# Kernel optimization log

Hardware: AMD Instinct MI355X
Metric: run time of the kernel (lower is better)

Reference implementation:

```python
import jax, jax.numpy as jnp
import numpy as np

EPS = 1e-5

def _layer_norm(x, gamma, beta):
    # LayerNorm over the last two dims [C, 128], matching nn.LayerNorm([C, 128])
    mean = jnp.mean(x, axis=(-2, -1), keepdims=True)
    var = jnp.var(x, axis=(-2, -1), keepdims=True)
    return (x - mean) * jax.lax.rsqrt(var + EPS) * gamma + beta


def setup_inputs() -> dict:
    key = jax.random.key(0)
    ks = jax.random.split(key, 7)
    B, C, N, L = 64, 1024, 128, 512
    W_SCALE = 0.02  # keep pre-softmax logits / activations in a sane range
    return {
        "X_in": jax.random.normal(ks[0], (B, C, N), jnp.float32),
        "T": jax.random.normal(ks[1], (B, C, L), jnp.float32),
        "Wq": jax.random.normal(ks[2], (C, C), jnp.float32) * W_SCALE,
        "Wk": jax.random.normal(ks[3], (C, C), jnp.float32) * W_SCALE,
        "Wv": jax.random.normal(ks[4], (C, C), jnp.float32) * W_SCALE,
        "Wf1": jax.random.normal(ks[5], (C, C), jnp.float32) * W_SCALE,
        "Wf2": jax.random.normal(ks[6], (C, C), jnp.float32) * W_SCALE,
        "gamma": jnp.ones((C, N), jnp.float32),
        "beta": jnp.zeros((C, N), jnp.float32),
    }


def reference(X_in, T, Wq, Wk, Wv, Wf1, Wf2, gamma, beta):
    C = Wq.shape[1]  # feature_map_cs (intended value of the buggy X_in.weight.shape[1])
    # 1x1 Conv1d == per-position channel matmul: weight [out, in]
    q = jnp.einsum('oc,bcn->bon', Wq, X_in)      # [B, C, N]
    k = jnp.einsum('oc,bcl->bol', Wk, T)         # [B, C, L]
    sim = jnp.einsum('bcn,bcl->bnl', q, k) / jnp.sqrt(jnp.float32(C))  # [B, N, L]
    attn = jax.nn.softmax(sim, axis=2)           # softmax over tokens L
    v = jnp.einsum('oc,bcl->bol', Wv, T)         # [B, C, L]
    ctx = jnp.einsum('bcl,bnl->bcn', v, attn)    # [B, C, N] == bmm(values, attn^T)
    X_out = _layer_norm(X_in + ctx, gamma, beta)
    h = jax.nn.relu(jnp.einsum('oc,bcn->bon', Wf1, X_out))
    ffn = jnp.einsum('oc,bcn->bon', Wf2, h)
    return _layer_norm(X_out + ffn, gamma, beta)
```

## Files before the change

### kernel.cpp

```cpp
#include <hip/hip_runtime.h>


using bf16   = __bf16;
using bf16x2 = __attribute__((ext_vector_type(2))) __bf16;
using bf16x4 = __attribute__((ext_vector_type(4))) __bf16;
using bf16x8 = __attribute__((ext_vector_type(8))) __bf16;
using f32x4  = __attribute__((ext_vector_type(4))) float;

static constexpr int  Bb = 64;
static constexpr int  Cc = 1024;
static constexpr int  Nn = 128;
static constexpr int  Ll = 512;
static constexpr long long PLANE = (long long)Cc * Nn;
static constexpr float INV_PLANE = 1.0f / 131072.0f;

__device__ __forceinline__ void gload_lds16(const void* g, void* l) {
    __builtin_amdgcn_global_load_lds(
        (__attribute__((address_space(1))) void*)g,
        (__attribute__((address_space(3))) void*)l,
        16, 0, 0);
}

__global__ void cast_w3(const float* __restrict__ a, const float* __restrict__ b,
                        const float* __restrict__ c,
                        bf16* __restrict__ oa, bf16* __restrict__ ob, bf16* __restrict__ oc) {
    const float* in; bf16* out;
    switch (blockIdx.y) {
        case 0: in = a; out = oa; break;
        case 1: in = b; out = ob; break;
        default: in = c; out = oc; break;
    }
    int i = blockIdx.x * 256 + threadIdx.x;
    float4 v = reinterpret_cast<const float4*>(in)[i];
    bf16x4 o = { (bf16)v.x, (bf16)v.y, (bf16)v.z, (bf16)v.w };
    reinterpret_cast<bf16x4*>(out)[i] = o;
}

template <bool DUAL>
__global__ void transpose_cast_f(const float* __restrict__ in, bf16* __restrict__ outT,
                                 bf16* __restrict__ outS, int R, int S) {
    __shared__ float tile[64][65];
    long long plane = (long long)R * S;
    in   += (long long)blockIdx.z * plane;
    outT += (long long)blockIdx.z * plane;
    if (DUAL) outS += (long long)blockIdx.z * plane;
    int s0 = blockIdx.x * 64, r0 = blockIdx.y * 64;
    int t = threadIdx.x;
    int rl = t >> 4;
    int sc = (t & 15) * 4;
    #pragma unroll
    for (int p = 0; p < 4; ++p) {
        int r = p * 16 + rl;
        float4 v = *(const float4*)(in + (long long)(r0 + r) * S + s0 + sc);
        *(float4*)&tile[r][sc] = v;
        if (DUAL) {
            bf16x4 o = { (bf16)v.x, (bf16)v.y, (bf16)v.z, (bf16)v.w };
            *(bf16x4*)(outS + (long long)(r0 + r) * S + s0 + sc) = o;
        }
    }
    __syncthreads();
    int sb = t >> 3;
    int rg = (t & 7) * 8;
    #pragma unroll
    for (int p = 0; p < 2; ++p) {
        int s = sb + p * 32;
        bf16x8 o;
        #pragma unroll
        for (int j = 0; j < 8; ++j) o[j] = (bf16)tile[rg + j][s];
        *(bf16x8*)(outT + (long long)(s0 + s) * R + r0 + rg) = o;
    }
}

#define GEMM_PROLOGUE_AND_LOOP(A_, Bt_, K_)                                        \
    __shared__ bf16 As[128 * 64];                                                  \
    __shared__ bf16 Bs[128 * 64];                                                  \
    const int n0   = blockIdx.x * 128;                                             \
    const int m0   = blockIdx.y * 128;                                             \
    const int t    = threadIdx.x;                                                  \
    const int lane = t & 63;                                                       \
    const int w    = t >> 6;                                                       \
    const int wr   = (w >> 1) * 64;                                                \
    const int wc   = (w & 1) * 64;                                                 \
    const int lr   = lane & 15;                                                    \
    const int hi4  = (lane >> 4) * 16;                                             \
    const int sw   = (lr & 7) << 4;                                                \
    const bf16* gA[4]; const bf16* gB[4]; int lo[4];                               \
    _Pragma("unroll")                                                              \
    for (int p = 0; p < 4; ++p) {                                                  \
        int o = w * 1024 + lane * 16 + p * 4096;                                   \
        int row = o >> 7;                                                          \
        int scol = ((o & 127) ^ ((row & 7) << 4)) >> 1;                            \
        lo[p] = o;                                                                 \
        gA[p] = A_  + (long long)(m0 + row) * K_ + scol;                           \
        gB[p] = Bt_ + (long long)(n0 + row) * K_ + scol;                           \
    }                                                                              \
    f32x4 acc[4][4] = {};                                                          \
    for (int k0 = 0; k0 < K_; k0 += 64) {                                          \
        _Pragma("unroll")                                                          \
        for (int p = 0; p < 4; ++p) gload_lds16(gA[p] + k0, (char*)As + lo[p]);    \
        _Pragma("unroll")                                                          \
        for (int p = 0; p < 4; ++p) gload_lds16(gB[p] + k0, (char*)Bs + lo[p]);    \
        __syncthreads();                                                           \
        _Pragma("unroll")                                                          \
        for (int kk = 0; kk < 2; ++kk) {                                           \
            bf16x8 af[4], bfr[4];                                                  \
            _Pragma("unroll")                                                      \
            for (int i = 0; i < 4; ++i) {                                          \
                int ra = wr + i * 16 + lr;                                         \
                int rb = wc + i * 16 + lr;                                         \
                af[i]  = *(const bf16x8*)((const char*)As +                        \
                          ((((ra << 7) + (kk << 6) + hi4)) ^ sw));                 \
                bfr[i] = *(const bf16x8*)((const char*)Bs +                        \
                          ((((rb << 7) + (kk << 6) + hi4)) ^ sw));                 \
            }                                                                      \
            _Pragma("unroll")                                                      \
            for (int mi = 0; mi < 4; ++mi)                                         \
                _Pragma("unroll")                                                  \
                for (int ni = 0; ni < 4; ++ni)                                     \
                    acc[mi][ni] = __builtin_amdgcn_mfma_f32_16x16x32_bf16(         \
                        af[mi], bfr[ni], acc[mi][ni], 0, 0, 0);                    \
        }                                                                          \
        __syncthreads();                                                           \
    }

template <typename OutT, bool RELU>
__global__ void __launch_bounds__(256, 2)
gemm_tn(const bf16* __restrict__ A, const bf16* __restrict__ Bt, OutT* __restrict__ C,
        int M, int N, int K, long long sA, long long sBt, long long sC, float scale) {
    A  += (long long)blockIdx.z * sA;
    Bt += (long long)blockIdx.z * sBt;
    C  += (long long)blockIdx.z * sC;
    GEMM_PROLOGUE_AND_LOOP(A, Bt, K)
    const int rbase = m0 + wr + (lane >> 4) * 4;
    const int cbase = n0 + wc + lr;
    #pragma unroll
    for (int mi = 0; mi < 4; ++mi)
        #pragma unroll
        for (int ni = 0; ni < 4; ++ni)
            #pragma unroll
            for (int r = 0; r < 4; ++r) {
                float v = acc[mi][ni][r] * scale;
                if (RELU) v = fmaxf(v, 0.0f);
                C[(long long)(rbase + mi * 16 + r) * N + (cbase + ni * 16)] = (OutT)v;
            }
}

__global__ void __launch_bounds__(256, 2)
gemm_ctx_ln1(const bf16* __restrict__ A , const bf16* __restrict__ Bt ,
             const float* __restrict__ X, float* __restrict__ Z1, float* __restrict__ partials,
             int K, long long sBt) {
    const int N = Nn;
    Bt += (long long)blockIdx.z * sBt;
    X  += (long long)blockIdx.z * PLANE;
    Z1 += (long long)blockIdx.z * PLANE;
    GEMM_PROLOGUE_AND_LOOP(A, Bt, K)
    const int rbase = m0 + wr + (lane >> 4) * 4;
    const int cbase = n0 + wc + lr;
    float s = 0.f, ss = 0.f;
    #pragma unroll
    for (int mi = 0; mi < 4; ++mi)
        #pragma unroll
        for (int ni = 0; ni < 4; ++ni)
            #pragma unroll
            for (int r = 0; r < 4; ++r) {
                long long idx = (long long)(rbase + mi * 16 + r) * N + (cbase + ni * 16);
                float zv = acc[mi][ni][r] + X[idx];
                Z1[idx] = zv;
                s += zv; ss += zv * zv;
            }
    #pragma unroll
    for (int off = 32; off; off >>= 1) { s += __shfl_xor(s, off); ss += __shfl_xor(ss, off); }
    __shared__ float red[8];
    if (lane == 0) { red[w] = s; red[4 + w] = ss; }
    __syncthreads();
    if (t == 0) {
        float S = red[0] + red[1] + red[2] + red[3];
        float SS = red[4] + red[5] + red[6] + red[7];
        float* p = partials + ((long long)blockIdx.z * 8 + blockIdx.y) * 2;
        p[0] = S; p[1] = SS;
    }
}

__global__ void __launch_bounds__(256, 2)
gemm_ffn_ln2(const bf16* __restrict__ A , const bf16* __restrict__ Bt ,
             const float* __restrict__ Xout, float* __restrict__ Z2, float* __restrict__ partials,
             int K, long long sA) {
    A    += (long long)blockIdx.z * sA;
    Xout += (long long)blockIdx.z * PLANE;
    Z2   += (long long)blockIdx.z * PLANE;
    GEMM_PROLOGUE_AND_LOOP(A, Bt, K)
    const int rbase = m0 + wr + (lane >> 4) * 4;
    const int cbase = n0 + wc + lr;
    float s = 0.f, ss = 0.f;
    #pragma unroll
    for (int mi = 0; mi < 4; ++mi)
        #pragma unroll
        for (int ni = 0; ni < 4; ++ni) {
            long long a = (long long)(cbase + ni * 16) * Nn + rbase + mi * 16;
            float4 xo = *(const float4*)(Xout + a);
            float4 zv = { acc[mi][ni][0] + xo.x, acc[mi][ni][1] + xo.y,
                          acc[mi][ni][2] + xo.z, acc[mi][ni][3] + xo.w };
            *(float4*)(Z2 + a) = zv;
            s  += zv.x + zv.y + zv.z + zv.w;
            ss += zv.x * zv.x + zv.y * zv.y + zv.z * zv.z + zv.w * zv.w;
        }
    #pragma unroll
    for (int off = 32; off; off >>= 1) { s += __shfl_xor(s, off); ss += __shfl_xor(ss, off); }
    __shared__ float red[8];
    if (lane == 0) { red[w] = s; red[4 + w] = ss; }
    __syncthreads();
    if (t == 0) {
        float S = red[0] + red[1] + red[2] + red[3];
        float SS = red[4] + red[5] + red[6] + red[7];
        float* p = partials + ((long long)blockIdx.z * 8 + blockIdx.x) * 2;
        p[0] = S; p[1] = SS;
    }
}

__global__ void softmax_rows_512(const float* __restrict__ sim, bf16* __restrict__ attn) {
    int row  = blockIdx.x * 4 + (threadIdx.x >> 6);
    int lane = threadIdx.x & 63;
    const float* p = sim + (long long)row * Ll + lane * 8;
    float4 a = *(const float4*)p;
    float4 b = *(const float4*)(p + 4);
    float v[8] = {a.x, a.y, a.z, a.w, b.x, b.y, b.z, b.w};
    float mx = v[0];
    #pragma unroll
    for (int j = 1; j < 8; ++j) mx = fmaxf(mx, v[j]);
    #pragma unroll
    for (int off = 32; off; off >>= 1) mx = fmaxf(mx, __shfl_xor(mx, off));
    float s = 0.f;
    #pragma unroll
    for (int j = 0; j < 8; ++j) { v[j] = __expf(v[j] - mx); s += v[j]; }
    #pragma unroll
    for (int off = 32; off; off >>= 1) s += __shfl_xor(s, off);
    float inv = 1.f / s;
    bf16x8 o;
    #pragma unroll
    for (int j = 0; j < 8; ++j) o[j] = (bf16)(v[j] * inv);
    *(bf16x8*)(attn + (long long)row * Ll + lane * 8) = o;
}

__global__ void ln1_norm_transpose(const float* __restrict__ Z1, const float* __restrict__ partials,
                                   const float* __restrict__ gamma, const float* __restrict__ beta,
                                   float* __restrict__ Xout, bf16* __restrict__ XoutT) {
    int b = blockIdx.z;
    float S = 0.f, SS = 0.f;
    #pragma unroll
    for (int j = 0; j < 8; ++j) {
        S  += partials[((long long)b * 8 + j) * 2];
        SS += partials[((long long)b * 8 + j) * 2 + 1];
    }
    float mean = S * INV_PLANE;
    float var  = SS * INV_PLANE - mean * mean;
    float rstd = rsqrtf(var + 1e-5f);
    __shared__ float tile[64][65];
    long long base = (long long)b * PLANE;
    int n0 = blockIdx.x * 64, c0 = blockIdx.y * 64;
    int t = threadIdx.x;
    int rl = t >> 4;
    int sc = (t & 15) * 4;
    #pragma unroll
    for (int p = 0; p < 4; ++p) {
        int r = p * 16 + rl;
        long long idx = (long long)(c0 + r) * Nn + n0 + sc;
        float4 z  = *(const float4*)(Z1 + base + idx);
        float4 g  = *(const float4*)(gamma + idx);
        float4 be = *(const float4*)(beta + idx);
        float4 o = {(z.x - mean) * rstd * g.x + be.x, (z.y - mean) * rstd * g.y + be.y,
                    (z.z - mean) * rstd * g.z + be.z, (z.w - mean) * rstd * g.w + be.w};
        *(float4*)(Xout + base + idx) = o;
        *(float4*)&tile[r][sc] = o;
    }
    __syncthreads();
    int sb = t >> 3;
    int rg = (t & 7) * 8;
    #pragma unroll
    for (int p = 0; p < 2; ++p) {
        int n = sb + p * 32;
        bf16x8 o;
        #pragma unroll
        for (int j = 0; j < 8; ++j) o[j] = (bf16)tile[rg + j][n];
        *(bf16x8*)(XoutT + base + (long long)(n0 + n) * Cc + c0 + rg) = o;
    }
}

__global__ void ln2_final(const float* __restrict__ Z2, const float* __restrict__ partials,
                          const float* __restrict__ gamma, const float* __restrict__ beta,
                          float* __restrict__ out) {
    int b = blockIdx.y;
    float S = 0.f, SS = 0.f;
    #pragma unroll
    for (int j = 0; j < 8; ++j) {
        S  += partials[((long long)b * 8 + j) * 2];
        SS += partials[((long long)b * 8 + j) * 2 + 1];
    }
    float mean = S * INV_PLANE;
    float var  = SS * INV_PLANE - mean * mean;
    float rstd = rsqrtf(var + 1e-5f);
    long long base = (long long)b * PLANE;
    int i = (blockIdx.x * 256 + threadIdx.x) * 4;
    float4 z  = *(const float4*)(Z2 + base + i);
    float4 g  = *(const float4*)(gamma + i);
    float4 be = *(const float4*)(beta + i);
    float4 o = {(z.x - mean) * rstd * g.x + be.x, (z.y - mean) * rstd * g.y + be.y,
                (z.z - mean) * rstd * g.z + be.z, (z.w - mean) * rstd * g.w + be.w};
    *(float4*)(out + base + i) = o;
}

extern "C" void kernel_launch(void* const* d_in, const int* in_sizes, int n_in,
                              void* d_out, int out_size, void* d_ws, size_t ws_size,
                              hipStream_t stream) {
    const float* X   = (const float*)d_in[0];
    const float* T   = (const float*)d_in[1];
    const float* Wq  = (const float*)d_in[2];
    const float* Wk  = (const float*)d_in[3];
    const float* Wv  = (const float*)d_in[4];
    const float* Wf1 = (const float*)d_in[5];
    const float* Wf2 = (const float*)d_in[6];
    const float* gamma = (const float*)d_in[7];
    const float* beta  = (const float*)d_in[8];
    float* out = (float*)d_out;
    char* ws = (char*)d_ws;
    const size_t MB = 1ull << 20;

    bf16* WvB  = (bf16*)(ws + 0 * MB);
    bf16* Wf1B = (bf16*)(ws + 2 * MB);
    bf16* Wf2B = (bf16*)(ws + 4 * MB);
    bf16* WqT  = (bf16*)(ws + 6 * MB);
    bf16* WkT  = (bf16*)(ws + 8 * MB);
    bf16* G2   = (bf16*)(ws + 10 * MB);
    bf16* Xt   = (bf16*)(ws + 12 * MB);
    bf16* Tt   = (bf16*)(ws + 28 * MB);
    float* Z1  = (float*)(ws + 28 * MB);
    float* Xout= (float*)(ws + 60 * MB);
    bf16* Tb   = (bf16*)(ws + 92 * MB);
    bf16* XoutT= (bf16*)(ws + 92 * MB);
    bf16* hT   = (bf16*)(ws + 108 * MB);
    bf16* e    = (bf16*)(ws + 156 * MB);
    float* Z2  = (float*)(ws + 156 * MB);
    float* sim = (float*)(ws + 172 * MB);
    bf16* attn = (bf16*)(ws + 188 * MB);
    bf16* u    = (bf16*)(ws + 196 * MB);
    float* pp1 = (float*)(ws + 212 * MB);
    float* pp2 = (float*)(ws + 212 * MB + 65536);

    dim3 blk256(256);

    cast_w3<<<dim3(Cc * Cc / 4 / 256, 3), blk256, 0, stream>>>(
        Wv, Wf1, Wf2, WvB, Wf1B, Wf2B);
    transpose_cast_f<false><<<dim3(16, 16, 1), blk256, 0, stream>>>(Wq, WqT, nullptr, Cc, Cc);
    transpose_cast_f<false><<<dim3(16, 16, 1), blk256, 0, stream>>>(Wk, WkT, nullptr, Cc, Cc);
    transpose_cast_f<false><<<dim3(Nn / 64, Cc / 64, Bb), blk256, 0, stream>>>(X, Xt, nullptr, Cc, Nn);
    transpose_cast_f<true><<<dim3(Ll / 64, Cc / 64, Bb), blk256, 0, stream>>>(T, Tt, Tb, Cc, Ll);

    gemm_tn<bf16, false><<<dim3(8, 8, 1), blk256, 0, stream>>>(
        WkT, WqT, G2, Cc, Cc, Cc, 0, 0, 0, 1.f);
    gemm_tn<bf16, false><<<dim3(8, 1, Bb), blk256, 0, stream>>>(
        Xt, G2, e, Nn, Cc, Cc, (long long)Nn * Cc, 0, (long long)Nn * Cc, 1.f);
    gemm_tn<float, false><<<dim3(4, 1, Bb), blk256, 0, stream>>>(
        e, Tt, sim, Nn, Ll, Cc, (long long)Nn * Cc, (long long)Ll * Cc,
        (long long)Nn * Ll, 0.03125f);
    softmax_rows_512<<<dim3(Bb * Nn / 4), blk256, 0, stream>>>(sim, attn);
    gemm_tn<bf16, false><<<dim3(8, 1, Bb), blk256, 0, stream>>>(
        attn, Tb, u, Nn, Cc, Ll, (long long)Nn * Ll, (long long)Cc * Ll,
        (long long)Nn * Cc, 1.f);
    gemm_ctx_ln1<<<dim3(1, 8, Bb), blk256, 0, stream>>>(
        WvB, u, X, Z1, pp1, Cc, (long long)Nn * Cc);
    ln1_norm_transpose<<<dim3(Nn / 64, Cc / 64, Bb), blk256, 0, stream>>>(
        Z1, pp1, gamma, beta, Xout, XoutT);
    gemm_tn<bf16, true><<<dim3(8, 1, Bb), blk256, 0, stream>>>(
        XoutT, Wf1B, hT, Nn, Cc, Cc, (long long)Nn * Cc, 0, (long long)Nn * Cc, 1.f);
    gemm_ffn_ln2<<<dim3(8, 1, Bb), blk256, 0, stream>>>(
        hT, Wf2B, Xout, Z2, pp2, Cc, (long long)Nn * Cc);
    ln2_final<<<dim3(128, Bb), blk256, 0, stream>>>(Z2, pp2, gamma, beta, out);
}
```

Baseline: 303.8 us.

## Fuse softmax into sim GEMM epilogue and recompute LN1 inside FFN2

The sim GEMM now writes exp(logits) as bf16 plus per-block row-sum partials, and the attention-value GEMM applies the reciprocal row sum in its epilogue. This removes the fp32 sim buffer and the separate softmax kernel. The fp32 Xout buffer is no longer written; the FFN2 epilogue recomputes LayerNorm-1 from Z1 and the stats. The Wq/Wk transposes are merged into one launch. Dropping max subtraction risks exp overflow for large logits.

```diff
diff --git a/kernel.cpp b/kernel.cpp
--- a/kernel.cpp
+++ b/kernel.cpp
@@ -68,6 +68,32 @@
         #pragma unroll
         for (int j = 0; j < 8; ++j) o[j] = (bf16)tile[rg + j][s];
         *(bf16x8*)(outT + (long long)(s0 + s) * R + r0 + rg) = o;
+    }
+}
+
+__global__ void transpose_cast_w2(const float* __restrict__ a, bf16* __restrict__ oa,
+                                  const float* __restrict__ b, bf16* __restrict__ ob) {
+    __shared__ float tile[64][65];
+    const float* in = blockIdx.z ? b : a;
+    bf16* out       = blockIdx.z ? ob : oa;
+    int s0 = blockIdx.x * 64, r0 = blockIdx.y * 64;
+    int t = threadIdx.x;
+    int rl = t >> 4, sc = (t & 15) * 4;
+    #pragma unroll
+    for (int p = 0; p < 4; ++p) {
+        int r = p * 16 + rl;
+        float4 v = *(const float4*)(in + (long long)(r0 + r) * Cc + s0 + sc);
+        *(float4*)&tile[r][sc] = v;
+    }
+    __syncthreads();
+    int sb = t >> 3, rg = (t & 7) * 8;
+    #pragma unroll
+    for (int p = 0; p < 2; ++p) {
+        int s = sb + p * 32;
+        bf16x8 o;
+        #pragma unroll
+        for (int j = 0; j < 8; ++j) o[j] = (bf16)tile[rg + j][s];
+        *(bf16x8*)(out + (long long)(s0 + s) * Cc + r0 + rg) = o;
     }
 }
 
@@ -146,6 +172,76 @@
 }
 
 __global__ void __launch_bounds__(256, 2)
+gemm_sim_exp(const bf16* __restrict__ A , const bf16* __restrict__ Bt ,
+             bf16* __restrict__ E, float* __restrict__ rspart, int K,
+             long long sA, long long sBt) {
+    A  += (long long)blockIdx.z * sA;
+    Bt += (long long)blockIdx.z * sBt;
+    E  += (long long)blockIdx.z * ((long long)Nn * Ll);
+    GEMM_PROLOGUE_AND_LOOP(A, Bt, K)
+    const int rbase = m0 + wr + (lane >> 4) * 4;
+    const int cbase = n0 + wc + lr;
+    __shared__ float rs[2][128];
+    float psum[4][4];
+    #pragma unroll
+    for (int mi = 0; mi < 4; ++mi)
+        #pragma unroll
+        for (int r = 0; r < 4; ++r) psum[mi][r] = 0.f;
+    #pragma unroll
+    for (int mi = 0; mi < 4; ++mi)
+        #pragma unroll
+        for (int ni = 0; ni < 4; ++ni)
+            #pragma unroll
+            for (int r = 0; r < 4; ++r) {
+                float ev = __expf(acc[mi][ni][r] * 0.03125f);
+                E[(long long)(rbase + mi * 16 + r) * Ll + (cbase + ni * 16)] = (bf16)ev;
+                psum[mi][r] += ev;
+            }
+    #pragma unroll
+    for (int mi = 0; mi < 4; ++mi)
+        #pragma unroll
+        for (int r = 0; r < 4; ++r) {
+            float v = psum[mi][r];
+            v += __shfl_xor(v, 1); v += __shfl_xor(v, 2);
+            v += __shfl_xor(v, 4); v += __shfl_xor(v, 8);
+            psum[mi][r] = v;
+        }
+    if (lr == 0) {
+        #pragma unroll
+        for (int mi = 0; mi < 4; ++mi)
+            #pragma unroll
+            for (int r = 0; r < 4; ++r)
+                rs[wc ? 1 : 0][wr + (lane >> 4) * 4 + mi * 16 + r] = psum[mi][r];
+    }
+    __syncthreads();
+    if (t < 128)
+        rspart[((long long)blockIdx.z * 4 + blockIdx.x) * 128 + t] = rs[0][t] + rs[1][t];
+}
+
+__global__ void __launch_bounds__(256, 2)
+gemm_u_scaled(const bf16* __restrict__ A , const bf16* __restrict__ Bt ,
+              bf16* __restrict__ C, const float* __restrict__ rspart, int K,
+              long long sA, long long sBt, long long sC) {
+    A  += (long long)blockIdx.z * sA;
+    Bt += (long long)blockIdx.z * sBt;
+    C  += (long long)blockIdx.z * sC;
+    const float* rp = rspart + (long long)blockIdx.z * 512;
+    GEMM_PROLOGUE_AND_LOOP(A, Bt, K)
+    const int rbase = m0 + wr + (lane >> 4) * 4;
+    const int cbase = n0 + wc + lr;
+    #pragma unroll
+    for (int mi = 0; mi < 4; ++mi)
+        #pragma unroll
+        for (int r = 0; r < 4; ++r) {
+            int row = rbase + mi * 16 + r;
+            float inv = 1.f / (rp[row] + rp[128 + row] + rp[256 + row] + rp[384 + row]);
+            #pragma unroll
+            for (int ni = 0; ni < 4; ++ni)
+                C[(long long)row * Cc + (cbase + ni * 16)] = (bf16)(acc[mi][ni][r] * inv);
+        }
+}
+
+__global__ void __launch_bounds__(256, 2)
 gemm_ctx_ln1(const bf16* __restrict__ A , const bf16* __restrict__ Bt ,
              const float* __restrict__ X, float* __restrict__ Z1, float* __restrict__ partials,
              int K, long long sBt) {
@@ -183,11 +279,21 @@
 
 __global__ void __launch_bounds__(256, 2)
 gemm_ffn_ln2(const bf16* __restrict__ A , const bf16* __restrict__ Bt ,
-             const float* __restrict__ Xout, float* __restrict__ Z2, float* __restrict__ partials,
+             const float* __restrict__ Z1, const float* __restrict__ pp1,
+             const float* __restrict__ gamma, const float* __restrict__ beta,
+             float* __restrict__ Z2, float* __restrict__ partials,
              int K, long long sA) {
-    A    += (long long)blockIdx.z * sA;
-    Xout += (long long)blockIdx.z * PLANE;
-    Z2   += (long long)blockIdx.z * PLANE;
+    A  += (long long)blockIdx.z * sA;
+    Z1 += (long long)blockIdx.z * PLANE;
+    Z2 += (long long)blockIdx.z * PLANE;
+    float S1 = 0.f, SS1 = 0.f;
+    #pragma unroll
+    for (int j = 0; j < 8; ++j) {
+        S1  += pp1[((long long)blockIdx.z * 8 + j) * 2];
+        SS1 += pp1[((long long)blockIdx.z * 8 + j) * 2 + 1];
+    }
+    const float mean1 = S1 * INV_PLANE;
+    const float rstd1 = rsqrtf(SS1 * INV_PLANE - mean1 * mean1 + 1e-5f);
     GEMM_PROLOGUE_AND_LOOP(A, Bt, K)
     const int rbase = m0 + wr + (lane >> 4) * 4;
     const int cbase = n0 + wc + lr;
@@ -197,7 +303,13 @@
         #pragma unroll
         for (int ni = 0; ni < 4; ++ni) {
             long long a = (long long)(cbase + ni * 16) * Nn + rbase + mi * 16;
-            float4 xo = *(const float4*)(Xout + a);
+            float4 z1v = *(const float4*)(Z1 + a);
+            float4 g  = *(const float4*)(gamma + a);
+            float4 be = *(const float4*)(beta + a);
+            float4 xo = {(z1v.x - mean1) * rstd1 * g.x + be.x,
+                         (z1v.y - mean1) * rstd1 * g.y + be.y,
+                         (z1v.z - mean1) * rstd1 * g.z + be.z,
+                         (z1v.w - mean1) * rstd1 * g.w + be.w};
             float4 zv = { acc[mi][ni][0] + xo.x, acc[mi][ni][1] + xo.y,
                           acc[mi][ni][2] + xo.z, acc[mi][ni][3] + xo.w };
             *(float4*)(Z2 + a) = zv;
@@ -217,33 +329,9 @@
     }
 }
 
-__global__ void softmax_rows_512(const float* __restrict__ sim, bf16* __restrict__ attn) {
-    int row  = blockIdx.x * 4 + (threadIdx.x >> 6);
-    int lane = threadIdx.x & 63;
-    const float* p = sim + (long long)row * Ll + lane * 8;
-    float4 a = *(const float4*)p;
-    float4 b = *(const float4*)(p + 4);
-    float v[8] = {a.x, a.y, a.z, a.w, b.x, b.y, b.z, b.w};
-    float mx = v[0];
-    #pragma unroll
-    for (int j = 1; j < 8; ++j) mx = fmaxf(mx, v[j]);
-    #pragma unroll
-    for (int off = 32; off; off >>= 1) mx = fmaxf(mx, __shfl_xor(mx, off));
-    float s = 0.f;
-    #pragma unroll
-    for (int j = 0; j < 8; ++j) { v[j] = __expf(v[j] - mx); s += v[j]; }
-    #pragma unroll
-    for (int off = 32; off; off >>= 1) s += __shfl_xor(s, off);
-    float inv = 1.f / s;
-    bf16x8 o;
-    #pragma unroll
-    for (int j = 0; j < 8; ++j) o[j] = (bf16)(v[j] * inv);
-    *(bf16x8*)(attn + (long long)row * Ll + lane * 8) = o;
-}
-
 __global__ void ln1_norm_transpose(const float* __restrict__ Z1, const float* __restrict__ partials,
                                    const float* __restrict__ gamma, const float* __restrict__ beta,
-                                   float* __restrict__ Xout, bf16* __restrict__ XoutT) {
+                                   bf16* __restrict__ XoutT) {
     int b = blockIdx.z;
     float S = 0.f, SS = 0.f;
     #pragma unroll
@@ -269,7 +357,6 @@
         float4 be = *(const float4*)(beta + idx);
         float4 o = {(z.x - mean) * rstd * g.x + be.x, (z.y - mean) * rstd * g.y + be.y,
                     (z.z - mean) * rstd * g.z + be.z, (z.w - mean) * rstd * g.w + be.w};
-        *(float4*)(Xout + base + idx) = o;
         *(float4*)&tile[r][sc] = o;
     }
     __syncthreads();
@@ -333,24 +420,22 @@
     bf16* Xt   = (bf16*)(ws + 12 * MB);
     bf16* Tt   = (bf16*)(ws + 28 * MB);
     float* Z1  = (float*)(ws + 28 * MB);
-    float* Xout= (float*)(ws + 60 * MB);
     bf16* Tb   = (bf16*)(ws + 92 * MB);
     bf16* XoutT= (bf16*)(ws + 92 * MB);
     bf16* hT   = (bf16*)(ws + 108 * MB);
     bf16* e    = (bf16*)(ws + 156 * MB);
     float* Z2  = (float*)(ws + 156 * MB);
-    float* sim = (float*)(ws + 172 * MB);
-    bf16* attn = (bf16*)(ws + 188 * MB);
+    bf16* E    = (bf16*)(ws + 188 * MB);
     bf16* u    = (bf16*)(ws + 196 * MB);
     float* pp1 = (float*)(ws + 212 * MB);
     float* pp2 = (float*)(ws + 212 * MB + 65536);
+    float* rsp = (float*)(ws + 213 * MB);
 
     dim3 blk256(256);
 
     cast_w3<<<dim3(Cc * Cc / 4 / 256, 3), blk256, 0, stream>>>(
         Wv, Wf1, Wf2, WvB, Wf1B, Wf2B);
-    transpose_cast_f<false><<<dim3(16, 16, 1), blk256, 0, stream>>>(Wq, WqT, nullptr, Cc, Cc);
-    transpose_cast_f<false><<<dim3(16, 16, 1), blk256, 0, stream>>>(Wk, WkT, nullptr, Cc, Cc);
+    transpose_cast_w2<<<dim3(16, 16, 2), blk256, 0, stream>>>(Wq, WqT, Wk, WkT);
     transpose_cast_f<false><<<dim3(Nn / 64, Cc / 64, Bb), blk256, 0, stream>>>(X, Xt, nullptr, Cc, Nn);
     transpose_cast_f<true><<<dim3(Ll / 64, Cc / 64, Bb), blk256, 0, stream>>>(T, Tt, Tb, Cc, Ll);
 
@@ -358,20 +443,17 @@
         WkT, WqT, G2, Cc, Cc, Cc, 0, 0, 0, 1.f);
     gemm_tn<bf16, false><<<dim3(8, 1, Bb), blk256, 0, stream>>>(
         Xt, G2, e, Nn, Cc, Cc, (long long)Nn * Cc, 0, (long long)Nn * Cc, 1.f);
-    gemm_tn<float, false><<<dim3(4, 1, Bb), blk256, 0, stream>>>(
-        e, Tt, sim, Nn, Ll, Cc, (long long)Nn * Cc, (long long)Ll * Cc,
-        (long long)Nn * Ll, 0.03125f);
-    softmax_rows_512<<<dim3(Bb * Nn / 4), blk256, 0, stream>>>(sim, attn);
-    gemm_tn<bf16, false><<<dim3(8, 1, Bb), blk256, 0, stream>>>(
-        attn, Tb, u, Nn, Cc, Ll, (long long)Nn * Ll, (long long)Cc * Ll,
-        (long long)Nn * Cc, 1.f);
+    gemm_sim_exp<<<dim3(4, 1, Bb), blk256, 0, stream>>>(
+        e, Tt, E, rsp, Cc, (long long)Nn * Cc, (long long)Ll * Cc);
+    gemm_u_scaled<<<dim3(8, 1, Bb), blk256, 0, stream>>>(
+        E, Tb, u, rsp, Ll, (long long)Nn * Ll, (long long)Cc * Ll, (long long)Nn * Cc);
     gemm_ctx_ln1<<<dim3(1, 8, Bb), blk256, 0, stream>>>(
         WvB, u, X, Z1, pp1, Cc, (long long)Nn * Cc);
     ln1_norm_transpose<<<dim3(Nn / 64, Cc / 64, Bb), blk256, 0, stream>>>(
-        Z1, pp1, gamma, beta, Xout, XoutT);
+        Z1, pp1, gamma, beta, XoutT);
     gemm_tn<bf16, true><<<dim3(8, 1, Bb), blk256, 0, stream>>>(
         XoutT, Wf1B, hT, Nn, Cc, Cc, (long long)Nn * Cc, 0, (long long)Nn * Cc, 1.f);
     gemm_ffn_ln2<<<dim3(8, 1, Bb), blk256, 0, stream>>>(
-        hT, Wf2B, Xout, Z2, pp2, Cc, (long long)Nn * Cc);
+        hT, Wf2B, Z1, pp1, gamma, beta, Z2, pp2, Cc, (long long)Nn * Cc);
     ln2_final<<<dim3(128, Bb), blk256, 0, stream>>>(Z2, pp2, gamma, beta, out);
 }
```

Result: faster. 292.8 us (-3.6%).
